# Kernel optimization log

Measured on AMD Instinct MI355X. Metric: run time of the kernel, lower is better.

Reference implementation:

```python
import jax, jax.numpy as jnp
import numpy as np

INPUT_DIM = 512
HEAD_NUM = 8
ATT_SIZE = 64
EPS = 1e-5


def layer_norm(x, g, b):
    mu = jnp.mean(x, axis=-1, keepdims=True)
    var = jnp.mean(jnp.square(x - mu), axis=-1, keepdims=True)
    return (x - mu) * jax.lax.rsqrt(var + EPS) * g + b


def setup_inputs() -> dict:
    key = jax.random.key(0)
    ks = jax.random.split(key, 10)
    D, H, A = INPUT_DIM, HEAD_NUM, ATT_SIZE
    HA = H * A
    s = lambda fan_in: 1.0 / np.sqrt(fan_in)
    x = jax.random.normal(ks[0], (32, 6, 256, D), dtype=jnp.float32)
    # Linear weights stored as [in, out] so y = x @ W + b (matches torch x @ W.T)
    Wq = jax.random.uniform(ks[1], (D, HA), jnp.float32, -s(D), s(D))
    bq = jnp.zeros((HA,), jnp.float32)
    Wk = jax.random.uniform(ks[2], (D, HA), jnp.float32, -s(D), s(D))
    bk = jnp.zeros((HA,), jnp.float32)
    Wv = jax.random.uniform(ks[3], (D, HA), jnp.float32, -s(D), s(D))
    bv = jnp.zeros((HA,), jnp.float32)
    Wo = jax.random.uniform(ks[4], (HA, D), jnp.float32, -s(HA), s(HA))
    bo = jnp.zeros((D,), jnp.float32)
    g1 = jnp.ones((D,), jnp.float32)
    b1 = jnp.zeros((D,), jnp.float32)
    Wd = jax.random.uniform(ks[5], (2 * D, D), jnp.float32, -s(2 * D), s(2 * D))
    bd = jnp.zeros((D,), jnp.float32)
    g2 = jnp.ones((D,), jnp.float32)
    b2 = jnp.zeros((D,), jnp.float32)
    return dict(x=x, Wq=Wq, bq=bq, Wk=Wk, bk=bk, Wv=Wv, bv=bv,
                Wo=Wo, bo=bo, g1=g1, b1=b1, Wd=Wd, bd=bd, g2=g2, b2=b2)


def reference(x, Wq, bq, Wk, bk, Wv, bv, Wo, bo, g1, b1, Wd, bd, g2, b2):
    B, M, P, D = x.shape
    H, A = HEAD_NUM, ATT_SIZE
    # QKV projections -> [B, M, H, P, A]
    q = (x @ Wq + bq).reshape(B, M, P, H, A).transpose(0, 1, 3, 2, 4)
    k = (x @ Wk + bk).reshape(B, M, P, H, A).transpose(0, 1, 3, 2, 4)
    v = (x @ Wv + bv).reshape(B, M, P, H, A).transpose(0, 1, 3, 2, 4)
    scores = jnp.einsum('bmhqa,bmhka->bmhqk', q, k) / jnp.sqrt(jnp.float32(A))
    attn = jax.nn.softmax(scores, axis=-1)
    z = jnp.einsum('bmhqk,bmhka->bmhqa', attn, v)
    z = z.transpose(0, 1, 3, 2, 4).reshape(B, M, P, H * A)
    z = jax.nn.relu(x + layer_norm(z @ Wo + bo, g1, b1))
    # patch merge (1/2 downsample)
    if P % 2:  # static shape check, fine under jit
        z = jnp.pad(z, ((0, 0), (0, 0), (0, 1), (0, 0)))
    merged = jnp.concatenate([z[:, :, 0::2, :], z[:, :, 1::2, :]], axis=-1)
    out = jax.nn.relu(layer_norm(merged @ Wd + bd, g2, b2))
    return out
```

## Files before the change

kernel.cpp:

```cpp
#include <hip/hip_runtime.h>
#include <hip/hip_bf16.h>
#include <stdint.h>


typedef __hip_bfloat16 bf16;
typedef __attribute__((ext_vector_type(8))) __bf16 bf16v8;
typedef __attribute__((ext_vector_type(4))) float f32x4;
typedef __attribute__((ext_vector_type(8))) short s16x8;
typedef __attribute__((ext_vector_type(4))) short s16x4;

static __device__ __forceinline__ void gl_lds16(const void* src, void* dst) {
  __builtin_amdgcn_global_load_lds((const __attribute__((address_space(1))) void*)src,
                                   (__attribute__((address_space(3))) void*)dst,
                                   16, 0, 0);
}

static __device__ __forceinline__ unsigned short f2bfu(float f) {
  return __builtin_bit_cast(unsigned short, __float2bfloat16(f));
}
static __device__ __forceinline__ float bfu2f(unsigned short u) {
  return __builtin_bit_cast(float, (unsigned int)u << 16);
}

__global__ __launch_bounds__(256) void conv_x_kernel(const float4* __restrict__ x,
                                                     s16x4* __restrict__ xb, int n4) {
  int stride = gridDim.x * 256;
  for (int i = blockIdx.x * 256 + threadIdx.x; i < n4; i += stride) {
    float4 v = x[i];
    s16x4 o;
    o[0] = (short)f2bfu(v.x); o[1] = (short)f2bfu(v.y);
    o[2] = (short)f2bfu(v.z); o[3] = (short)f2bfu(v.w);
    xb[i] = o;
  }
}

__global__ __launch_bounds__(256) void conv_w_kernel(
    const float* __restrict__ Wq, const float* __restrict__ Wk, const float* __restrict__ Wv,
    const float* __restrict__ Wo, const float* __restrict__ Wd,
    const float* __restrict__ bq, const float* __restrict__ bk, const float* __restrict__ bv,
    bf16* __restrict__ wqkv_t, bf16* __restrict__ wo_t, bf16* __restrict__ wd_t,
    float* __restrict__ bqkv) {
  int o = blockIdx.x * 256 + threadIdx.x;
  if (o < 786432) {
    int j = o >> 9, kk = o & 511;
    const float* W = (j < 512) ? Wq : (j < 1024) ? Wk : Wv;
    wqkv_t[o] = __float2bfloat16(W[kk * 512 + (j & 511)]);
  } else if (o < 1048576) {
    int o2 = o - 786432; int j = o2 >> 9, kk = o2 & 511;
    wo_t[o2] = __float2bfloat16(Wo[kk * 512 + j]);
  } else if (o < 1572864) {
    int o3 = o - 1048576; int j = o3 >> 10, kk = o3 & 1023;
    wd_t[o3] = __float2bfloat16(Wd[kk * 512 + j]);
  } else if (o < 1574400) {
    int o4 = o - 1572864;
    const float* b = (o4 < 512) ? bq : (o4 < 1024) ? bk : bv;
    bqkv[o4] = b[o4 & 511];
  }
}

template<int EPI, int AMODE>
__global__ __launch_bounds__(256, 2) void gemm128(
    const bf16* __restrict__ A, const bf16* __restrict__ Bt,
    const float* __restrict__ bias, int K, int nN,
    bf16* __restrict__ oq, bf16* __restrict__ ok, bf16* __restrict__ ovt,
    bf16* __restrict__ obf) {
  __shared__ __align__(16) char smem[65536];
  const int tid = threadIdx.x;
  const int wave = tid >> 6, lane = tid & 63;
  const int wr = wave >> 1, wc = wave & 1;
  const int lane15 = lane & 15, g = lane >> 4;

  const int cpx = gridDim.x >> 3;
  const int lin = (blockIdx.x & 7) * cpx + (blockIdx.x >> 3);
  const int tileM = (lin / nN) * 128, tileN = (lin % nN) * 128;

  const int iters = K >> 7;

  auto stage = [&](int tau, int q) {
    char* dstb = smem + ((tau & 1) << 15) + ((q >> 1) << 14) + ((q & 1) << 13);
#pragma unroll
    for (int u = 0; u < 2; ++u) {
      int slot = u * 256 + tid;
      int r = slot >> 3;
      int c = (slot & 7) ^ (r & 7);
      int kpos = tau * 64 + c * 8;
      if (q < 2) {
        int mr = tileM + ((q & 1) << 6) + r;
        const bf16* s;
        if (AMODE == 0) {
          s = A + (size_t)mr * K + kpos;
        } else {
          int bm = mr >> 7, pp = mr & 127;
          s = A + (size_t)(bm * 256 + pp * 2 + (kpos >> 9)) * 512 + (kpos & 511);
        }
        gl_lds16(s, dstb + slot * 16);
      } else {
        int nr = tileN + ((q & 1) << 6) + r;
        gl_lds16(Bt + (size_t)nr * K + kpos, dstb + slot * 16);
      }
    }
  };

  f32x4 acc[4][4] = {};
  bf16v8 areg[2][2], breg[2][2][2];
  const int swl = (lane15 & 7);

  stage(0, 0); stage(0, 1); stage(0, 2); stage(0, 3);
  stage(1, 0); stage(1, 1);
  asm volatile("s_waitcnt vmcnt(4)" ::: "memory");
  __builtin_amdgcn_s_barrier();

  for (int it = 0; it < iters; ++it) {
    const bool last = (it == iters - 1);
#pragma unroll
    for (int p = 0; p < 8; ++p) {
      const int buf = p >> 2;
      const int mh = (p >> 1) & 1, nh = p & 1;
      char* Ab = smem + (buf << 15);
      char* Bb = Ab + 16384;
      if (nh == 0) {
#pragma unroll
        for (int f = 0; f < 2; ++f) {
          int row = wr * 64 + mh * 32 + f * 16 + lane15;
#pragma unroll
          for (int ks = 0; ks < 2; ++ks)
            areg[f][ks] = *(const bf16v8*)(Ab + row * 128 + (((ks * 4 + g) ^ swl) << 4));
        }
      }
      if ((p & 3) <= 1) {
#pragma unroll
        for (int n = 0; n < 2; ++n) {
          int row = wc * 64 + nh * 32 + n * 16 + lane15;
#pragma unroll
          for (int ks = 0; ks < 2; ++ks)
            breg[nh][n][ks] = *(const bf16v8*)(Bb + row * 128 + (((ks * 4 + g) ^ swl) << 4));
        }
      }
      if (p == 0)      { stage(2 * it + 1, 2); stage(2 * it + 1, 3); }
      else if (p == 3) { if (!last) { stage(2 * it + 2, 0); stage(2 * it + 2, 1); } }
      else if (p == 4) { if (!last) { stage(2 * it + 2, 2); stage(2 * it + 2, 3); } }
      else if (p == 7) { if (!last) { stage(2 * it + 3, 0); stage(2 * it + 3, 1); } }
      __builtin_amdgcn_s_setprio(1);
#pragma unroll
      for (int ks = 0; ks < 2; ++ks)
#pragma unroll
        for (int f = 0; f < 2; ++f)
#pragma unroll
          for (int n = 0; n < 2; ++n)
            acc[mh * 2 + f][nh * 2 + n] = __builtin_amdgcn_mfma_f32_16x16x32_bf16(
                areg[f][ks], breg[nh][n][ks], acc[mh * 2 + f][nh * 2 + n], 0, 0, 0);
      __builtin_amdgcn_s_setprio(0);
      if (p == 2 || p == 6) {
        asm volatile("s_waitcnt lgkmcnt(0)" ::: "memory");
        __builtin_amdgcn_s_barrier();
      } else if (p == 3) {
        if (last) { asm volatile("s_waitcnt vmcnt(0) lgkmcnt(0)" ::: "memory"); }
        else      { asm volatile("s_waitcnt vmcnt(4) lgkmcnt(0)" ::: "memory"); }
        __builtin_amdgcn_s_barrier();
      } else if (p == 7) {
        if (last) { asm volatile("s_waitcnt lgkmcnt(0)" ::: "memory"); }
        else      { asm volatile("s_waitcnt vmcnt(4) lgkmcnt(0)" ::: "memory"); }
        __builtin_amdgcn_s_barrier();
      }
    }
  }

  const int rowstart = tileM + wr * 64;
  if (EPI == 0 && tileN >= 1024) {
    const int cb = tileN + wc * 64;
    const int hh = (cb - 1024) >> 6;
    const int bmq = rowstart >> 8, p0off = rowstart & 255;
    char* slab = smem + wave * 8192;
#pragma unroll
    for (int fm = 0; fm < 4; ++fm) {
#pragma unroll
      for (int fn = 0; fn < 4; ++fn) {
        float bb = bias[cb + fn * 16 + lane15];
        int a = fn * 16 + lane15;
#pragma unroll
        for (int i = 0; i < 4; ++i) {
          int pl = fm * 16 + g * 4 + i;
          *(bf16*)(slab + a * 128 + ((pl * 2) ^ ((a & 7) << 4))) =
              __float2bfloat16(acc[fm][fn][i] + bb);
        }
      }
    }
    asm volatile("" ::: "memory");
    bf16* vdst = ovt + ((size_t)(bmq * 8 + hh) << 14) + p0off;
#pragma unroll
    for (int r = 0; r < 8; ++r) {
      int a = r * 8 + (lane >> 3);
      int ps = lane & 7;
      s16x8 vv = *(const s16x8*)(slab + a * 128 + ((ps * 16) ^ ((a & 7) << 4)));
      *(s16x8*)(vdst + a * 256 + ps * 8) = vv;
    }
  } else {
    char* slab = smem + wave * 8192;
#pragma unroll
    for (int fm = 0; fm < 4; ++fm) {
#pragma unroll
      for (int fn = 0; fn < 4; ++fn) {
        int col = tileN + wc * 64 + fn * 16 + lane15;
        float bb = bias[col];
        int lb = (fn * 16 + lane15) * 2;
#pragma unroll
        for (int i = 0; i < 4; ++i) {
          int pl = fm * 16 + g * 4 + i;
          *(bf16*)(slab + pl * 128 + (lb ^ ((((pl >> 2) & 3)) << 5))) =
              __float2bfloat16(acc[fm][fn][i] + bb);
        }
      }
    }
    asm volatile("" ::: "memory");
    bf16* dst; int ldc2;
    if (EPI == 0) {
      int cb = tileN + wc * 64;
      int hh = (cb >> 6) & 7;
      bf16* base = (cb < 512) ? oq : ok;
      dst = base + (((size_t)((rowstart >> 8) * 8 + hh)) << 14) + (rowstart & 255) * 64;
      ldc2 = 64;
    } else {
      dst = obf + (size_t)rowstart * 512 + tileN + wc * 64;
      ldc2 = 512;
    }
#pragma unroll
    for (int r = 0; r < 8; ++r) {
      int s = r * 64 + lane;
      int pl = s >> 3, sl = s & 7;
      s16x8 vv = *(const s16x8*)(slab + pl * 128 + ((sl * 16) ^ ((((pl >> 2) & 3)) << 5)));
      *(s16x8*)(dst + (size_t)pl * ldc2 + sl * 8) = vv;
    }
  }
}

__global__ __launch_bounds__(256) void attn_kernel(const bf16* __restrict__ q,
                                                   const bf16* __restrict__ k,
                                                   const bf16* __restrict__ vt,
                                                   bf16* __restrict__ z) {
  __shared__ __align__(16) char smem[81920];
  const int tid = threadIdx.x, wave = tid >> 6, lane = tid & 63;
  const int lane15 = lane & 15, g = lane >> 4;
  const int qc = blockIdx.x, hh = blockIdx.y, bm = blockIdx.z;
  const int bh = bm * 8 + hh;
  const bf16* kbase = k + ((size_t)bh << 14);
  const bf16* vbase = vt + ((size_t)bh << 14);
  const bf16* qbase = q + ((size_t)bh << 14) + (qc * 64 + wave * 16) * 64;

#pragma unroll
  for (int i = 0; i < 8; ++i) {
    int s = i * 256 + tid;
    int kr = s >> 3, ksp = s & 7;
    gl_lds16(kbase + kr * 64 + (ksp ^ (kr & 7)) * 8, smem + s * 16);
    int ar = s >> 5, asp = s & 31;
    gl_lds16(vbase + ar * 256 + (asp ^ (ar & 7)) * 8, smem + 32768 + s * 16);
  }
  bf16v8 qf[2];
#pragma unroll
  for (int kk = 0; kk < 2; ++kk)
    qf[kk] = *(const bf16v8*)(qbase + lane15 * 64 + kk * 32 + g * 8);
  __syncthreads();

  f32x4 sacc[16] = {};
#pragma unroll
  for (int tl = 0; tl < 16; ++tl) {
    int key = tl * 16 + lane15;
    int rb = key * 128, swk = (key & 7) << 4;
#pragma unroll
    for (int kk = 0; kk < 2; ++kk) {
      bf16v8 kf = *(const bf16v8*)(smem + rb + (((kk * 4 + g) * 16) ^ swk));
      sacc[tl] = __builtin_amdgcn_mfma_f32_16x16x32_bf16(qf[kk], kf, sacc[tl], 0, 0, 0);
    }
  }

  float mx[4], sm[4], rcp[4];
#pragma unroll
  for (int i = 0; i < 4; ++i) mx[i] = sacc[0][i];
#pragma unroll
  for (int tl = 1; tl < 16; ++tl)
#pragma unroll
    for (int i = 0; i < 4; ++i) mx[i] = fmaxf(mx[i], sacc[tl][i]);
#pragma unroll
  for (int i = 0; i < 4; ++i) {
    mx[i] = fmaxf(mx[i], __shfl_xor(mx[i], 1));
    mx[i] = fmaxf(mx[i], __shfl_xor(mx[i], 2));
    mx[i] = fmaxf(mx[i], __shfl_xor(mx[i], 4));
    mx[i] = fmaxf(mx[i], __shfl_xor(mx[i], 8));
    sm[i] = 0.f;
  }
#pragma unroll
  for (int tl = 0; tl < 16; ++tl)
#pragma unroll
    for (int i = 0; i < 4; ++i) {
      float e = __expf((sacc[tl][i] - mx[i]) * 0.125f);
      sacc[tl][i] = e; sm[i] += e;
    }
#pragma unroll
  for (int i = 0; i < 4; ++i) {
    sm[i] += __shfl_xor(sm[i], 1);
    sm[i] += __shfl_xor(sm[i], 2);
    sm[i] += __shfl_xor(sm[i], 4);
    sm[i] += __shfl_xor(sm[i], 8);
    rcp[i] = 1.0f / sm[i];
  }

  char* pbase = smem + 65536 + wave * 4096;
  f32x4 oacc[4] = {};
#pragma unroll
  for (int h2 = 0; h2 < 2; ++h2) {
#pragma unroll
    for (int t8 = 0; t8 < 8; ++t8) {
      int tl = h2 * 8 + t8;
#pragma unroll
      for (int i = 0; i < 4; ++i) {
        int r = g * 4 + i;
        int c2 = t8 * 16 + lane15;
        *(bf16*)(pbase + r * 256 + ((c2 * 2) ^ ((r & 7) << 4))) =
            __float2bfloat16(sacc[tl][i] * rcp[i]);
      }
    }
    asm volatile("" ::: "memory");
#pragma unroll
    for (int k2 = 0; k2 < 4; ++k2) {
      int ks = h2 * 4 + k2;
      bf16v8 pf = *(const bf16v8*)(pbase + lane15 * 256 +
                                   ((k2 * 64 + g * 16) ^ ((lane15 & 7) << 4)));
#pragma unroll
      for (int at = 0; at < 4; ++at) {
        int a = at * 16 + lane15;
        bf16v8 vf = *(const bf16v8*)(smem + 32768 + a * 512 +
                                     ((ks * 64 + g * 16) ^ ((a & 7) << 4)));
        oacc[at] = __builtin_amdgcn_mfma_f32_16x16x32_bf16(pf, vf, oacc[at], 0, 0, 0);
      }
    }
    asm volatile("" ::: "memory");
  }

  int trow = bm * 256 + qc * 64 + wave * 16;
#pragma unroll
  for (int at = 0; at < 4; ++at)
#pragma unroll
    for (int i = 0; i < 4; ++i)
      z[(size_t)(trow + g * 4 + i) * 512 + hh * 64 + at * 16 + lane15] =
          __float2bfloat16(oacc[at][i]);
}

static __device__ __forceinline__ float wredsum(float v) {
  v += __shfl_xor(v, 1);  v += __shfl_xor(v, 2);  v += __shfl_xor(v, 4);
  v += __shfl_xor(v, 8);  v += __shfl_xor(v, 16); v += __shfl_xor(v, 32);
  return v;
}

__global__ __launch_bounds__(256) void ln_res_kernel(const bf16* __restrict__ y1,
                                                     const float* __restrict__ x,
                                                     const float* __restrict__ g1,
                                                     const float* __restrict__ b1,
                                                     bf16* __restrict__ z2) {
  const int wave = threadIdx.x >> 6, lane = threadIdx.x & 63;
  const int row = blockIdx.x * 4 + wave;
  const size_t base = (size_t)row * 512 + lane * 8;
  s16x8 yv = *(const s16x8*)(y1 + base);
  float f[8];
#pragma unroll
  for (int j = 0; j < 8; ++j) f[j] = bfu2f((unsigned short)yv[j]);
  float s = 0.f, s2 = 0.f;
#pragma unroll
  for (int j = 0; j < 8; ++j) { s += f[j]; s2 += f[j] * f[j]; }
  s = wredsum(s); s2 = wredsum(s2);
  float mu = s * (1.f / 512.f);
  float var = s2 * (1.f / 512.f) - mu * mu;
  float rs = rsqrtf(var + 1e-5f);
  float4 x0 = *(const float4*)(x + base);
  float4 x1 = *(const float4*)(x + base + 4);
  float xa[8] = {x0.x, x0.y, x0.z, x0.w, x1.x, x1.y, x1.z, x1.w};
  float ga[8], ba[8];
#pragma unroll
  for (int j = 0; j < 8; ++j) { ga[j] = g1[lane * 8 + j]; ba[j] = b1[lane * 8 + j]; }
  s16x8 ov;
#pragma unroll
  for (int j = 0; j < 8; ++j) {
    float v = xa[j] + (f[j] - mu) * rs * ga[j] + ba[j];
    ov[j] = (short)f2bfu(fmaxf(v, 0.f));
  }
  *(s16x8*)(z2 + base) = ov;
}

__global__ __launch_bounds__(256) void ln_out_kernel(const bf16* __restrict__ y2,
                                                     const float* __restrict__ g2,
                                                     const float* __restrict__ b2,
                                                     float* __restrict__ out) {
  const int wave = threadIdx.x >> 6, lane = threadIdx.x & 63;
  const int row = blockIdx.x * 4 + wave;
  const size_t base = (size_t)row * 512 + lane * 8;
  s16x8 yv = *(const s16x8*)(y2 + base);
  float f[8];
#pragma unroll
  for (int j = 0; j < 8; ++j) f[j] = bfu2f((unsigned short)yv[j]);
  float s = 0.f, s2 = 0.f;
#pragma unroll
  for (int j = 0; j < 8; ++j) { s += f[j]; s2 += f[j] * f[j]; }
  s = wredsum(s); s2 = wredsum(s2);
  float mu = s * (1.f / 512.f);
  float var = s2 * (1.f / 512.f) - mu * mu;
  float rs = rsqrtf(var + 1e-5f);
  float o[8];
#pragma unroll
  for (int j = 0; j < 8; ++j)
    o[j] = fmaxf((f[j] - mu) * rs * g2[lane * 8 + j] + b2[lane * 8 + j], 0.f);
  float4 w0 = {o[0], o[1], o[2], o[3]};
  float4 w1 = {o[4], o[5], o[6], o[7]};
  *(float4*)(out + base) = w0;
  *(float4*)(out + base + 4) = w1;
}

extern "C" void kernel_launch(void* const* d_in, const int* in_sizes, int n_in,
                              void* d_out, int out_size, void* d_ws, size_t ws_size,
                              hipStream_t stream) {
  const float* x  = (const float*)d_in[0];
  const float* Wq = (const float*)d_in[1];
  const float* bq = (const float*)d_in[2];
  const float* Wk = (const float*)d_in[3];
  const float* bk = (const float*)d_in[4];
  const float* Wv = (const float*)d_in[5];
  const float* bv = (const float*)d_in[6];
  const float* Wo = (const float*)d_in[7];
  const float* bo = (const float*)d_in[8];
  const float* g1 = (const float*)d_in[9];
  const float* b1 = (const float*)d_in[10];
  const float* Wd = (const float*)d_in[11];
  const float* bd = (const float*)d_in[12];
  const float* g2 = (const float*)d_in[13];
  const float* b2 = (const float*)d_in[14];

  char* ws = (char*)d_ws;
  const size_t SEG = 50331648;
  bf16*  xb   = (bf16*)(ws);
  bf16*  qb   = (bf16*)(ws + SEG);
  bf16*  kb   = (bf16*)(ws + 2 * SEG);
  bf16*  vtb  = (bf16*)(ws + 3 * SEG);
  bf16*  wqkv = (bf16*)(ws + 4 * SEG);
  bf16*  wot  = (bf16*)(ws + 4 * SEG + 1572864);
  bf16*  wdt  = (bf16*)(ws + 4 * SEG + 2097152);
  float* bqkv = (float*)(ws + 4 * SEG + 3145728);
  bf16*  zb   = xb;
  bf16*  y1   = qb;
  bf16*  z2   = kb;
  bf16*  y2   = vtb;

  conv_x_kernel<<<4096, 256, 0, stream>>>((const float4*)x, (s16x4*)xb, 25165824 / 4);
  conv_w_kernel<<<6150, 256, 0, stream>>>(Wq, Wk, Wv, Wo, Wd, bq, bk, bv,
                                          wqkv, wot, wdt, bqkv);
  gemm128<0, 0><<<4608, 256, 0, stream>>>(xb, wqkv, bqkv, 512, 12,
                                          qb, kb, vtb, nullptr);
  attn_kernel<<<dim3(4, 8, 192), 256, 0, stream>>>(qb, kb, vtb, zb);
  gemm128<1, 0><<<1536, 256, 0, stream>>>(zb, wot, bo, 512, 4,
                                          nullptr, nullptr, nullptr, y1);
  ln_res_kernel<<<12288, 256, 0, stream>>>(y1, x, g1, b1, z2);
  gemm128<1, 1><<<768, 256, 0, stream>>>(z2, wdt, bd, 1024, 4,
                                         nullptr, nullptr, nullptr, y2);
  ln_out_kernel<<<6144, 256, 0, stream>>>(y2, g2, b2, (float*)d_out);
}
```

Measured before the change: 317.3 us.

## Process all 256 queries per attention block to reuse staged K/V tiles

Each attention block now handles every query row for one (batch, head) pair instead of a 64-row chunk, with each wave looping over four 16-row fragments. This removes the fourfold reloading of K and V into LDS across query-chunk blocks and cuts the grid by four. It also adds s_setprio around the MFMA sections, and hoists the x loads in the layernorm-residual kernel ahead of the reduction. The cost is fewer blocks for latency hiding, plus higher register use from holding Q fragments for all four row groups.

Measured after the change: 307.0 us. -3.2%, faster.

```diff
diff --git a/kernel.cpp b/kernel.cpp
--- a/kernel.cpp
+++ b/kernel.cpp
@@ -240,11 +240,10 @@
   __shared__ __align__(16) char smem[81920];
   const int tid = threadIdx.x, wave = tid >> 6, lane = tid & 63;
   const int lane15 = lane & 15, g = lane >> 4;
-  const int qc = blockIdx.x, hh = blockIdx.y, bm = blockIdx.z;
+  const int hh = blockIdx.x, bm = blockIdx.y;
   const int bh = bm * 8 + hh;
   const bf16* kbase = k + ((size_t)bh << 14);
   const bf16* vbase = vt + ((size_t)bh << 14);
-  const bf16* qbase = q + ((size_t)bh << 14) + (qc * 64 + wave * 16) * 64;
 
 #pragma unroll
   for (int i = 0; i < 8; ++i) {
@@ -254,94 +253,106 @@
     int ar = s >> 5, asp = s & 31;
     gl_lds16(vbase + ar * 256 + (asp ^ (ar & 7)) * 8, smem + 32768 + s * 16);
   }
-  bf16v8 qf[2];
-#pragma unroll
-  for (int kk = 0; kk < 2; ++kk)
-    qf[kk] = *(const bf16v8*)(qbase + lane15 * 64 + kk * 32 + g * 8);
+  bf16v8 qf[4][2];
+#pragma unroll
+  for (int fr = 0; fr < 4; ++fr) {
+    const bf16* qb2 = q + ((size_t)bh << 14) + (wave * 64 + fr * 16) * 64;
+#pragma unroll
+    for (int kk = 0; kk < 2; ++kk)
+      qf[fr][kk] = *(const bf16v8*)(qb2 + lane15 * 64 + kk * 32 + g * 8);
+  }
   __syncthreads();
 
-  f32x4 sacc[16] = {};
-#pragma unroll
-  for (int tl = 0; tl < 16; ++tl) {
-    int key = tl * 16 + lane15;
-    int rb = key * 128, swk = (key & 7) << 4;
-#pragma unroll
-    for (int kk = 0; kk < 2; ++kk) {
-      bf16v8 kf = *(const bf16v8*)(smem + rb + (((kk * 4 + g) * 16) ^ swk));
-      sacc[tl] = __builtin_amdgcn_mfma_f32_16x16x32_bf16(qf[kk], kf, sacc[tl], 0, 0, 0);
-    }
-  }
-
-  float mx[4], sm[4], rcp[4];
-#pragma unroll
-  for (int i = 0; i < 4; ++i) mx[i] = sacc[0][i];
-#pragma unroll
-  for (int tl = 1; tl < 16; ++tl)
-#pragma unroll
-    for (int i = 0; i < 4; ++i) mx[i] = fmaxf(mx[i], sacc[tl][i]);
-#pragma unroll
-  for (int i = 0; i < 4; ++i) {
-    mx[i] = fmaxf(mx[i], __shfl_xor(mx[i], 1));
-    mx[i] = fmaxf(mx[i], __shfl_xor(mx[i], 2));
-    mx[i] = fmaxf(mx[i], __shfl_xor(mx[i], 4));
-    mx[i] = fmaxf(mx[i], __shfl_xor(mx[i], 8));
-    sm[i] = 0.f;
-  }
-#pragma unroll
-  for (int tl = 0; tl < 16; ++tl)
+  char* pbase = smem + 65536 + wave * 4096;
+
+#pragma unroll
+  for (int fr = 0; fr < 4; ++fr) {
+    f32x4 sacc[16] = {};
+    __builtin_amdgcn_s_setprio(1);
+#pragma unroll
+    for (int tl = 0; tl < 16; ++tl) {
+      int key = tl * 16 + lane15;
+      int rb = key * 128, swk = (key & 7) << 4;
+#pragma unroll
+      for (int kk = 0; kk < 2; ++kk) {
+        bf16v8 kf = *(const bf16v8*)(smem + rb + (((kk * 4 + g) * 16) ^ swk));
+        sacc[tl] = __builtin_amdgcn_mfma_f32_16x16x32_bf16(qf[fr][kk], kf, sacc[tl], 0, 0, 0);
+      }
+    }
+    __builtin_amdgcn_s_setprio(0);
+
+    float mx[4], sm[4], rcp[4];
+#pragma unroll
+    for (int i = 0; i < 4; ++i) mx[i] = sacc[0][i];
+#pragma unroll
+    for (int tl = 1; tl < 16; ++tl)
+#pragma unroll
+      for (int i = 0; i < 4; ++i) mx[i] = fmaxf(mx[i], sacc[tl][i]);
 #pragma unroll
     for (int i = 0; i < 4; ++i) {
-      float e = __expf((sacc[tl][i] - mx[i]) * 0.125f);
-      sacc[tl][i] = e; sm[i] += e;
-    }
-#pragma unroll
-  for (int i = 0; i < 4; ++i) {
-    sm[i] += __shfl_xor(sm[i], 1);
-    sm[i] += __shfl_xor(sm[i], 2);
-    sm[i] += __shfl_xor(sm[i], 4);
-    sm[i] += __shfl_xor(sm[i], 8);
-    rcp[i] = 1.0f / sm[i];
-  }
-
-  char* pbase = smem + 65536 + wave * 4096;
-  f32x4 oacc[4] = {};
-#pragma unroll
-  for (int h2 = 0; h2 < 2; ++h2) {
-#pragma unroll
-    for (int t8 = 0; t8 < 8; ++t8) {
-      int tl = h2 * 8 + t8;
+      mx[i] = fmaxf(mx[i], __shfl_xor(mx[i], 1));
+      mx[i] = fmaxf(mx[i], __shfl_xor(mx[i], 2));
+      mx[i] = fmaxf(mx[i], __shfl_xor(mx[i], 4));
+      mx[i] = fmaxf(mx[i], __shfl_xor(mx[i], 8));
+      sm[i] = 0.f;
+    }
+#pragma unroll
+    for (int tl = 0; tl < 16; ++tl)
 #pragma unroll
       for (int i = 0; i < 4; ++i) {
-        int r = g * 4 + i;
-        int c2 = t8 * 16 + lane15;
-        *(bf16*)(pbase + r * 256 + ((c2 * 2) ^ ((r & 7) << 4))) =
-            __float2bfloat16(sacc[tl][i] * rcp[i]);
-      }
-    }
-    asm volatile("" ::: "memory");
-#pragma unroll
-    for (int k2 = 0; k2 < 4; ++k2) {
-      int ks = h2 * 4 + k2;
-      bf16v8 pf = *(const bf16v8*)(pbase + lane15 * 256 +
-                                   ((k2 * 64 + g * 16) ^ ((lane15 & 7) << 4)));
-#pragma unroll
-      for (int at = 0; at < 4; ++at) {
-        int a = at * 16 + lane15;
-        bf16v8 vf = *(const bf16v8*)(smem + 32768 + a * 512 +
-                                     ((ks * 64 + g * 16) ^ ((a & 7) << 4)));
-        oacc[at] = __builtin_amdgcn_mfma_f32_16x16x32_bf16(pf, vf, oacc[at], 0, 0, 0);
-      }
-    }
-    asm volatile("" ::: "memory");
-  }
-
-  int trow = bm * 256 + qc * 64 + wave * 16;
-#pragma unroll
-  for (int at = 0; at < 4; ++at)
-#pragma unroll
-    for (int i = 0; i < 4; ++i)
-      z[(size_t)(trow + g * 4 + i) * 512 + hh * 64 + at * 16 + lane15] =
-          __float2bfloat16(oacc[at][i]);
+        float e = __expf((sacc[tl][i] - mx[i]) * 0.125f);
+        sacc[tl][i] = e; sm[i] += e;
+      }
+#pragma unroll
+    for (int i = 0; i < 4; ++i) {
+      sm[i] += __shfl_xor(sm[i], 1);
+      sm[i] += __shfl_xor(sm[i], 2);
+      sm[i] += __shfl_xor(sm[i], 4);
+      sm[i] += __shfl_xor(sm[i], 8);
+      rcp[i] = 1.0f / sm[i];
+    }
+
+    f32x4 oacc[4] = {};
+#pragma unroll
+    for (int h2 = 0; h2 < 2; ++h2) {
+#pragma unroll
+      for (int t8 = 0; t8 < 8; ++t8) {
+        int tl = h2 * 8 + t8;
+#pragma unroll
+        for (int i = 0; i < 4; ++i) {
+          int r = g * 4 + i;
+          int c2 = t8 * 16 + lane15;
+          *(bf16*)(pbase + r * 256 + ((c2 * 2) ^ ((r & 7) << 4))) =
+              __float2bfloat16(sacc[tl][i] * rcp[i]);
+        }
+      }
+      asm volatile("" ::: "memory");
+      __builtin_amdgcn_s_setprio(1);
+#pragma unroll
+      for (int k2 = 0; k2 < 4; ++k2) {
+        int ks = h2 * 4 + k2;
+        bf16v8 pf = *(const bf16v8*)(pbase + lane15 * 256 +
+                                     ((k2 * 64 + g * 16) ^ ((lane15 & 7) << 4)));
+#pragma unroll
+        for (int at = 0; at < 4; ++at) {
+          int a = at * 16 + lane15;
+          bf16v8 vf = *(const bf16v8*)(smem + 32768 + a * 512 +
+                                       ((ks * 64 + g * 16) ^ ((a & 7) << 4)));
+          oacc[at] = __builtin_amdgcn_mfma_f32_16x16x32_bf16(pf, vf, oacc[at], 0, 0, 0);
+        }
+      }
+      __builtin_amdgcn_s_setprio(0);
+      asm volatile("" ::: "memory");
+    }
+
+    int trow = bm * 256 + wave * 64 + fr * 16;
+#pragma unroll
+    for (int at = 0; at < 4; ++at)
+#pragma unroll
+      for (int i = 0; i < 4; ++i)
+        z[(size_t)(trow + g * 4 + i) * 512 + hh * 64 + at * 16 + lane15] =
+            __float2bfloat16(oacc[at][i]);
+  }
 }
 
 static __device__ __forceinline__ float wredsum(float v) {
@@ -359,6 +370,8 @@
   const int row = blockIdx.x * 4 + wave;
   const size_t base = (size_t)row * 512 + lane * 8;
   s16x8 yv = *(const s16x8*)(y1 + base);
+  f32x4 x0 = *(const f32x4*)(x + base);
+  f32x4 x1 = *(const f32x4*)(x + base + 4);
   float f[8];
 #pragma unroll
   for (int j = 0; j < 8; ++j) f[j] = bfu2f((unsigned short)yv[j]);
@@ -369,9 +382,7 @@
   float mu = s * (1.f / 512.f);
   float var = s2 * (1.f / 512.f) - mu * mu;
   float rs = rsqrtf(var + 1e-5f);
-  float4 x0 = *(const float4*)(x + base);
-  float4 x1 = *(const float4*)(x + base + 4);
-  float xa[8] = {x0.x, x0.y, x0.z, x0.w, x1.x, x1.y, x1.z, x1.w};
+  float xa[8] = {x0[0], x0[1], x0[2], x0[3], x1[0], x1[1], x1[2], x1[3]};
   float ga[8], ba[8];
 #pragma unroll
   for (int j = 0; j < 8; ++j) { ga[j] = g1[lane * 8 + j]; ba[j] = b1[lane * 8 + j]; }
@@ -451,7 +462,7 @@
                                           wqkv, wot, wdt, bqkv);
   gemm128<0, 0><<<4608, 256, 0, stream>>>(xb, wqkv, bqkv, 512, 12,
                                           qb, kb, vtb, nullptr);
-  attn_kernel<<<dim3(4, 8, 192), 256, 0, stream>>>(qb, kb, vtb, zb);
+  attn_kernel<<<dim3(8, 192), 256, 0, stream>>>(qb, kb, vtb, zb);
   gemm128<1, 0><<<1536, 256, 0, stream>>>(zb, wot, bo, 512, 4,
                                           nullptr, nullptr, nullptr, y1);
   ln_res_kernel<<<12288, 256, 0, stream>>>(y1, x, g1, b1, z2);
```
